# Kernel tuning notes

Measured on AMD Instinct MI355X. Metric: run time of the kernel, lower is better.

The kernel has to match this reference:

```python
import jax, jax.numpy as jnp
import numpy as np
from functools import partial

V, CTX, D, H, L, FF = 50257, 1024, 768, 12, 12, 3072
DH = D // H
EPS = 1e-5


def _ln(x, g, b):
    m = jnp.mean(x, axis=-1, keepdims=True)
    v = jnp.mean(jnp.square(x - m), axis=-1, keepdims=True)
    return (x - m) * jax.lax.rsqrt(v + EPS) * g + b


def setup_inputs() -> dict:
    key = jax.random.key(0)
    ks = jax.random.split(key, 8)
    s = 0.02
    return {
        "input_ids": jax.random.randint(ks[0], (2, 1024), 0, V),
        "token_emb": jax.random.normal(ks[1], (V, D), jnp.float32) * s,
        "pos_emb": jax.random.normal(ks[2], (CTX, D), jnp.float32) * s,
        "ln1_g": jnp.ones((L, D), jnp.float32),
        "ln1_b": jnp.zeros((L, D), jnp.float32),
        "qkv_w": jax.random.normal(ks[3], (L, 3 * D, D), jnp.float32) * s,
        "out_w": jax.random.normal(ks[4], (L, D, D), jnp.float32) * (s / np.sqrt(2 * L)),
        "ln2_g": jnp.ones((L, D), jnp.float32),
        "ln2_b": jnp.zeros((L, D), jnp.float32),
        "ff1_w": jax.random.normal(ks[5], (L, FF, D), jnp.float32) * s,
        "ff2_w": jax.random.normal(ks[6], (L, D, FF), jnp.float32) * s,
        "lnf_g": jnp.ones((D,), jnp.float32),
        "lnf_b": jnp.zeros((D,), jnp.float32),
    }


def reference(input_ids, token_emb, pos_emb, ln1_g, ln1_b, qkv_w, out_w,
              ln2_g, ln2_b, ff1_w, ff2_w, lnf_g, lnf_b):
    B, T = input_ids.shape
    x = token_emb[input_ids] + pos_emb[:T]  # [B,T,D]
    causal = jnp.tril(jnp.ones((T, T), bool))  # True = keep
    scale = 1.0 / np.sqrt(DH)

    def block(x, p):
        g1, b1, wqkv, wo, g2, b2, w1, w2 = p
        h = _ln(x, g1, b1)
        qkv = h @ wqkv.T  # [B,T,3D]
        q, k, v = jnp.split(qkv, 3, axis=-1)
        q = q.reshape(B, T, H, DH).transpose(0, 2, 1, 3)
        k = k.reshape(B, T, H, DH).transpose(0, 2, 1, 3)
        v = v.reshape(B, T, H, DH).transpose(0, 2, 1, 3)
        scores = jnp.einsum('bhqd,bhkd->bhqk', q, k) * scale
        scores = jnp.where(causal, scores, -jnp.inf)
        w = jax.nn.softmax(scores, axis=-1)
        o = jnp.einsum('bhqk,bhkd->bhqd', w, v)
        o = o.transpose(0, 2, 1, 3).reshape(B, T, D) @ wo.T
        x = x + o
        h2 = _ln(x, g2, b2)
        ff = jax.nn.gelu(h2 @ w1.T, approximate=False) @ w2.T
        return x + ff, None

    params = (ln1_g, ln1_b, qkv_w, out_w, ln2_g, ln2_b, ff1_w, ff2_w)
    x, _ = jax.lax.scan(block, x, params)
    x = _ln(x, lnf_g, lnf_b)
    logits = x @ token_emb.T  # tied lm head
    return logits
```

## Files before the change

kernel.cpp:

```cpp
#include <hip/hip_runtime.h>
#include <hip/hip_bf16.h>
#include <math.h>

#define D_MODEL 768
#define NHEAD 12
#define DHEAD 64
#define NLAYER 12
#define FF_DIM 3072
#define SEQ 1024
#define TOKENS 2048
#define VOCAB 50257

typedef short bf16x8 __attribute__((ext_vector_type(8)));
typedef float f32x4 __attribute__((ext_vector_type(4)));
typedef unsigned short u16x4 __attribute__((ext_vector_type(4)));
typedef unsigned short u16x8 __attribute__((ext_vector_type(8)));

__device__ inline unsigned short f2bf(float f) {
    union { float f; unsigned u; } un;
    un.f = f;
    unsigned u = un.u;
    u += 0x7fffu + ((u >> 16) & 1u);
    return (unsigned short)(u >> 16);
}

__device__ inline void gl_lds16(const void* g, void* l) {
    __builtin_amdgcn_global_load_lds(
        (const __attribute__((address_space(1))) unsigned int*)g,
        (__attribute__((address_space(3))) unsigned int*)l, 16, 0, 0);
}

__global__ __launch_bounds__(256) void cvt_kernel(const float* __restrict__ s,
                                                  unsigned short* __restrict__ d,
                                                  long n4) {
    long i = (long)blockIdx.x * 256 + threadIdx.x;
    long stride = (long)gridDim.x * 256;
    for (; i < n4; i += stride) {
        f32x4 v = ((const f32x4*)s)[i];
        u16x4 r;
        r[0] = f2bf(v[0]); r[1] = f2bf(v[1]); r[2] = f2bf(v[2]); r[3] = f2bf(v[3]);
        ((u16x4*)d)[i] = r;
    }
}

__global__ __launch_bounds__(256) void embed_kernel(const int* __restrict__ ids,
                                                    const float* __restrict__ tok,
                                                    const float* __restrict__ pos,
                                                    float* __restrict__ x) {
    int i = blockIdx.x * 256 + threadIdx.x;
    int row = i / D_MODEL;
    int d = i - row * D_MODEL;
    int t = row & (SEQ - 1);
    x[i] = tok[(long)ids[row] * D_MODEL + d] + pos[(long)t * D_MODEL + d];
}

__global__ __launch_bounds__(256) void ln_kernel(const float* __restrict__ x,
                                                 const float* __restrict__ g,
                                                 const float* __restrict__ b,
                                                 unsigned short* __restrict__ out) {
    int row = blockIdx.x;
    int tid = threadIdx.x;
    const float* xr = x + (long)row * D_MODEL;
    float v0 = xr[tid], v1 = xr[tid + 256], v2 = xr[tid + 512];
    __shared__ float sm[4];
    float s = v0 + v1 + v2;
    #pragma unroll
    for (int off = 32; off; off >>= 1) s += __shfl_xor(s, off);
    if ((tid & 63) == 0) sm[tid >> 6] = s;
    __syncthreads();
    float mean = (sm[0] + sm[1] + sm[2] + sm[3]) * (1.f / D_MODEL);
    __syncthreads();
    float d0 = v0 - mean, d1 = v1 - mean, d2 = v2 - mean;
    s = d0 * d0 + d1 * d1 + d2 * d2;
    #pragma unroll
    for (int off = 32; off; off >>= 1) s += __shfl_xor(s, off);
    if ((tid & 63) == 0) sm[tid >> 6] = s;
    __syncthreads();
    float var = (sm[0] + sm[1] + sm[2] + sm[3]) * (1.f / D_MODEL);
    float rs = rsqrtf(var + 1e-5f);
    unsigned short* orow = out + (long)row * D_MODEL;
    orow[tid]       = f2bf(d0 * rs * g[tid]       + b[tid]);
    orow[tid + 256] = f2bf(d1 * rs * g[tid + 256] + b[tid + 256]);
    orow[tid + 512] = f2bf(d2 * rs * g[tid + 512] + b[tid + 512]);
}

#define GM_NONE 0
#define GM_RES  1
#define GM_GELU 2
#define GM_QKV  3

template<int WM, int WN, int MODE, bool SWZ>
__global__ __launch_bounds__(256) void gemm_bf16(
        const unsigned short* __restrict__ A, const unsigned short* __restrict__ W,
        int M, int N, int K,
        float* __restrict__ Cf, unsigned short* __restrict__ Cb,
        const float* __restrict__ RES,
        unsigned short* __restrict__ P1, unsigned short* __restrict__ P2) {
    constexpr int BM = WM * 32, BN = WN * 32;
    __shared__ unsigned short lA[2][BM * 64];
    __shared__ unsigned short lB[2][BN * 64];

    int tid = threadIdx.x;
    int lane = tid & 63, wv = tid >> 6;
    int wr = wv >> 1, wc = wv & 1;
    int lr = lane & 15, kq = lane >> 4;

    int mtile, ntile;
    if (SWZ) {
        int lb = blockIdx.y * gridDim.x + blockIdx.x;
        int g = lb >> 3, r8 = lb & 7;
        mtile = g % gridDim.x;
        ntile = (g / gridDim.x) * 8 + r8;
        if (ntile * BN >= N) return;
    } else {
        mtile = blockIdx.x;
        ntile = blockIdx.y;
    }
    int row0 = mtile * BM;
    int col0 = ntile * BN;

    int srow_in = tid >> 3;
    int ssp = tid & 7;
    int skg = ssp ^ (srow_in & 7);
    int lbase = ((tid & ~63)) << 3;

    f32x4 acc[WM][WN];
    #pragma unroll
    for (int m = 0; m < WM; m++)
        #pragma unroll
        for (int n = 0; n < WN; n++) acc[m][n] = (f32x4){0.f, 0.f, 0.f, 0.f};

    auto stage = [&](int buf, int kt) {
        #pragma unroll
        for (int i = 0; i < BM / 32; i++) {
            int row = i * 32 + srow_in;
            gl_lds16(A + (size_t)(row0 + row) * K + kt + skg * 8,
                     &lA[buf][i * 2048 + lbase]);
        }
        #pragma unroll
        for (int i = 0; i < BN / 32; i++) {
            int row = i * 32 + srow_in;
            int srow = col0 + row;
            if (srow >= N) srow = N - 1;
            gl_lds16(W + (size_t)srow * K + kt + skg * 8,
                     &lB[buf][i * 2048 + lbase]);
        }
    };

    stage(0, 0);
    __syncthreads();
    int nt = K >> 6;
    int cur = 0;
    for (int t = 0; t < nt; t++) {
        if (t + 1 < nt) stage(cur ^ 1, (t + 1) << 6);
        #pragma unroll
        for (int kk = 0; kk < 2; kk++) {
            int kg = kk * 4 + kq;
            bf16x8 af[WM], bfr[WN];
            #pragma unroll
            for (int m = 0; m < WM; m++) {
                int row = wr * (WM * 16) + m * 16 + lr;
                af[m] = *(const bf16x8*)&lA[cur][row * 64 + ((kg ^ (row & 7)) << 3)];
            }
            #pragma unroll
            for (int n = 0; n < WN; n++) {
                int row = wc * (WN * 16) + n * 16 + lr;
                bfr[n] = *(const bf16x8*)&lB[cur][row * 64 + ((kg ^ (row & 7)) << 3)];
            }
            #pragma unroll
            for (int m = 0; m < WM; m++)
                #pragma unroll
                for (int n = 0; n < WN; n++)
                    acc[m][n] = __builtin_amdgcn_mfma_f32_16x16x32_bf16(af[m], bfr[n], acc[m][n], 0, 0, 0);
        }
        __syncthreads();
        cur ^= 1;
    }

    #pragma unroll
    for (int m = 0; m < WM; m++) {
        int r0 = row0 + wr * (WM * 16) + m * 16 + (kq << 2);
        #pragma unroll
        for (int n = 0; n < WN; n++) {
            int c = col0 + wc * (WN * 16) + n * 16 + lr;
            if (c < N) {
                #pragma unroll
                for (int j = 0; j < 4; j++) {
                    int r = r0 + j;
                    size_t idx = (size_t)r * N + c;
                    float v = acc[m][n][j];
                    if (MODE == GM_RES) {
                        Cf[idx] = v + RES[idx];
                    } else if (MODE == GM_GELU) {
                        Cb[idx] = f2bf(0.5f * v * (1.f + erff(v * 0.70710678118f)));
                    } else if (MODE == GM_QKV) {
                        int bb = r >> 10, t = r & 1023;
                        if (c < D_MODEL) {
                            int h = c >> 6, dh = c & 63;
                            P1[(((size_t)(bb * NHEAD + h) * SEQ) + t) * 64 + dh] = f2bf(v * 0.125f);
                        } else if (c < 2 * D_MODEL) {
                            int cc = c - D_MODEL;
                            int h = cc >> 6, dh = cc & 63;
                            P2[(((size_t)(bb * NHEAD + h) * SEQ) + t) * 64 + dh] = f2bf(v);
                        } else {
                            Cb[(size_t)r * D_MODEL + (c - 2 * D_MODEL)] = f2bf(v);
                        }
                    } else {
                        Cf[idx] = v;
                    }
                }
            }
        }
    }
}

__global__ __launch_bounds__(256) void vprep_kernel(const unsigned short* __restrict__ Vrow,
                                                    unsigned short* __restrict__ Vt) {
    __shared__ unsigned short T[64][66];
    int b = blockIdx.z, h = blockIdx.y, t0 = blockIdx.x * 64;
    int tid = threadIdx.x;
    int tin = tid >> 2, seg = tid & 3;
    const unsigned short* src = Vrow + ((size_t)(b * SEQ) + t0 + tin) * D_MODEL
                                + h * 64 + seg * 16;
    u16x8 a0 = *(const u16x8*)src;
    u16x8 a1 = *(const u16x8*)(src + 8);
    #pragma unroll
    for (int e = 0; e < 8; e++) { T[tin][seg * 16 + e] = a0[e]; T[tin][seg * 16 + 8 + e] = a1[e]; }
    __syncthreads();
    int dh = tid >> 2;
    unsigned short* dst = Vt + ((size_t)(b * NHEAD + h) * 64 + dh) * SEQ + t0 + seg * 16;
    u16x8 o0, o1;
    #pragma unroll
    for (int e = 0; e < 8; e++) o0[e] = T[seg * 16 + e][dh];
    #pragma unroll
    for (int e = 0; e < 8; e++) o1[e] = T[seg * 16 + 8 + e][dh];
    *(u16x8*)dst = o0;
    *(u16x8*)(dst + 8) = o1;
}

__global__ __launch_bounds__(128) void attn_mfma(const unsigned short* __restrict__ Qb,
                                                 const unsigned short* __restrict__ Kb,
                                                 const unsigned short* __restrict__ Vt,
                                                 unsigned short* __restrict__ att) {
    int b = blockIdx.z, h = blockIdx.y, pr = blockIdx.x;
    int tid = threadIdx.x, l = tid & 63, w = tid >> 6;
    int lr = l & 15, hg = l >> 4;
    int hk8 = hg * 8, hg4 = hg * 4;
    size_t bh = (size_t)b * NHEAD + h;
    const unsigned short* Qp = Qb + bh * SEQ * 64;
    const unsigned short* Kp = Kb + bh * SEQ * 64;
    const unsigned short* Vp = Vt + bh * 64 * SEQ;

    __shared__ float sm_m[2][2][16], sm_l[2][2][16];
    __shared__ float sm_o[2][2][16][64];
    __shared__ unsigned short pl[2][1024];
    unsigned short* Pw = &pl[w][0];

    #pragma unroll
    for (int ti = 0; ti < 2; ti++) {
        int tile = ti ? (63 - pr) : pr;
        int q0 = tile * 16;
        bf16x8 qf0 = *(const bf16x8*)(Qp + (size_t)(q0 + lr) * 64 + hk8);
        bf16x8 qf1 = *(const bf16x8*)(Qp + (size_t)(q0 + lr) * 64 + 32 + hk8);
        f32x4 O[4];
        #pragma unroll
        for (int dt = 0; dt < 4; dt++) O[dt] = (f32x4){0.f, 0.f, 0.f, 0.f};
        f32x4 mrun = (f32x4){-1e30f, -1e30f, -1e30f, -1e30f};
        f32x4 lrun = (f32x4){0.f, 0.f, 0.f, 0.f};
        int nch = (tile >> 2) + 1;

        for (int c = w; c < nch; c += 2) {
            int k0 = c * 64;
            f32x4 S[4];
            #pragma unroll
            for (int kt = 0; kt < 4; kt++) {
                S[kt] = (f32x4){0.f, 0.f, 0.f, 0.f};
                bf16x8 kf = *(const bf16x8*)(Kp + (size_t)(k0 + kt * 16 + lr) * 64 + hk8);
                S[kt] = __builtin_amdgcn_mfma_f32_16x16x32_bf16(qf0, kf, S[kt], 0, 0, 0);
                kf = *(const bf16x8*)(Kp + (size_t)(k0 + kt * 16 + lr) * 64 + 32 + hk8);
                S[kt] = __builtin_amdgcn_mfma_f32_16x16x32_bf16(qf1, kf, S[kt], 0, 0, 0);
            }
            if (c == nch - 1) {
                #pragma unroll
                for (int kt = 0; kt < 4; kt++)
                    #pragma unroll
                    for (int j = 0; j < 4; j++)
                        S[kt][j] = (k0 + kt * 16 + lr <= q0 + hg4 + j) ? S[kt][j] : -3.0e38f;
            }
            f32x4 rm;
            #pragma unroll
            for (int j = 0; j < 4; j++)
                rm[j] = fmaxf(fmaxf(S[0][j], S[1][j]), fmaxf(S[2][j], S[3][j]));
            #pragma unroll
            for (int msk = 1; msk <= 8; msk <<= 1)
                #pragma unroll
                for (int j = 0; j < 4; j++)
                    rm[j] = fmaxf(rm[j], __shfl_xor(rm[j], msk));
            f32x4 mn, corr, rs;
            #pragma unroll
            for (int j = 0; j < 4; j++) {
                mn[j] = fmaxf(mrun[j], rm[j]);
                corr[j] = __expf(mrun[j] - mn[j]);
                rs[j] = 0.f;
            }
            #pragma unroll
            for (int kt = 0; kt < 4; kt++)
                #pragma unroll
                for (int j = 0; j < 4; j++) {
                    float p = __expf(S[kt][j] - mn[j]);
                    S[kt][j] = p;
                    rs[j] += p;
                }
            #pragma unroll
            for (int msk = 1; msk <= 8; msk <<= 1)
                #pragma unroll
                for (int j = 0; j < 4; j++)
                    rs[j] += __shfl_xor(rs[j], msk);
            #pragma unroll
            for (int j = 0; j < 4; j++) {
                lrun[j] = lrun[j] * corr[j] + rs[j];
                mrun[j] = mn[j];
            }
            #pragma unroll
            for (int dt = 0; dt < 4; dt++)
                #pragma unroll
                for (int j = 0; j < 4; j++) O[dt][j] *= corr[j];
            #pragma unroll
            for (int kt = 0; kt < 4; kt++) {
                int cc = kt * 16 + lr;
                int slot = cc >> 3, off = cc & 7;
                #pragma unroll
                for (int j = 0; j < 4; j++) {
                    int r = hg4 + j;
                    Pw[r * 64 + ((slot ^ (r & 7)) << 3) + off] = f2bf(S[kt][j]);
                }
            }
            asm volatile("s_waitcnt lgkmcnt(0)" ::: "memory");
            bf16x8 pf0 = *(const bf16x8*)&Pw[lr * 64 + ((hg ^ (lr & 7)) << 3)];
            bf16x8 pf1 = *(const bf16x8*)&Pw[lr * 64 + (((4 + hg) ^ (lr & 7)) << 3)];
            #pragma unroll
            for (int dt = 0; dt < 4; dt++) {
                bf16x8 vf = *(const bf16x8*)(Vp + (size_t)(dt * 16 + lr) * SEQ + k0 + hk8);
                O[dt] = __builtin_amdgcn_mfma_f32_16x16x32_bf16(pf0, vf, O[dt], 0, 0, 0);
                vf = *(const bf16x8*)(Vp + (size_t)(dt * 16 + lr) * SEQ + k0 + 32 + hk8);
                O[dt] = __builtin_amdgcn_mfma_f32_16x16x32_bf16(pf1, vf, O[dt], 0, 0, 0);
            }
        }
        if (lr == 0) {
            #pragma unroll
            for (int j = 0; j < 4; j++) {
                sm_m[w][ti][hg4 + j] = mrun[j];
                sm_l[w][ti][hg4 + j] = lrun[j];
            }
        }
        #pragma unroll
        for (int dt = 0; dt < 4; dt++)
            #pragma unroll
            for (int j = 0; j < 4; j++)
                sm_o[w][ti][hg4 + j][dt * 16 + lr] = O[dt][j];
    }
    __syncthreads();
    {
        int tile = w ? (63 - pr) : pr;
        int q0 = tile * 16;
        #pragma unroll
        for (int j = 0; j < 4; j++) {
            int r = hg4 + j;
            float m0 = sm_m[0][w][r], m1 = sm_m[1][w][r];
            float M = fmaxf(m0, m1);
            float e0 = __expf(m0 - M), e1 = __expf(m1 - M);
            float L = sm_l[0][w][r] * e0 + sm_l[1][w][r] * e1;
            float invL = 1.f / L;
            unsigned short* orow = att + ((size_t)(b * SEQ + q0 + r)) * D_MODEL + h * 64;
            #pragma unroll
            for (int dt = 0; dt < 4; dt++) {
                float o = sm_o[0][w][r][dt * 16 + lr] * e0 + sm_o[1][w][r][dt * 16 + lr] * e1;
                orow[dt * 16 + lr] = f2bf(o * invL);
            }
        }
    }
}

extern "C" void kernel_launch(void* const* d_in, const int* in_sizes, int n_in,
                              void* d_out, int out_size, void* d_ws, size_t ws_size,
                              hipStream_t stream) {
    const int*   input_ids = (const int*)d_in[0];
    const float* token_emb = (const float*)d_in[1];
    const float* pos_emb   = (const float*)d_in[2];
    const float* ln1_g     = (const float*)d_in[3];
    const float* ln1_b     = (const float*)d_in[4];
    const float* qkv_w     = (const float*)d_in[5];
    const float* out_w     = (const float*)d_in[6];
    const float* ln2_g     = (const float*)d_in[7];
    const float* ln2_b     = (const float*)d_in[8];
    const float* ff1_w     = (const float*)d_in[9];
    const float* ff2_w     = (const float*)d_in[10];
    const float* lnf_g     = (const float*)d_in[11];
    const float* lnf_b     = (const float*)d_in[12];
    float* out = (float*)d_out;

    const size_t SZ_QKV_L = (size_t)3 * D_MODEL * D_MODEL;
    const size_t SZ_OUT_L = (size_t)D_MODEL * D_MODEL;
    const size_t SZ_FF1_L = (size_t)FF_DIM * D_MODEL;
    const size_t SZ_FF2_L = (size_t)D_MODEL * FF_DIM;
    const size_t SZ_TOK   = (size_t)VOCAB * D_MODEL;

    char* base = (char*)d_ws;
    size_t off = 0;
    auto alloc = [&](size_t bytes) -> char* {
        char* p = base + off;
        off = (off + bytes + 255) & ~(size_t)255;
        return p;
    };

    float* x              = (float*)alloc((size_t)TOKENS * D_MODEL * 4);
    unsigned short* hb    = (unsigned short*)alloc((size_t)TOKENS * D_MODEL * 2);
    unsigned short* attb  = (unsigned short*)alloc((size_t)TOKENS * D_MODEL * 2);
    unsigned short* ffab  = (unsigned short*)alloc((size_t)TOKENS * FF_DIM * 2);
    unsigned short* Qb    = (unsigned short*)alloc((size_t)TOKENS * D_MODEL * 2);
    unsigned short* Kb    = (unsigned short*)alloc((size_t)TOKENS * D_MODEL * 2);
    unsigned short* Vrow  = (unsigned short*)alloc((size_t)TOKENS * D_MODEL * 2);
    unsigned short* Vtb   = (unsigned short*)alloc((size_t)TOKENS * D_MODEL * 2);

    size_t act_end = off;
    size_t full_need = act_end + 2 * (NLAYER * (SZ_QKV_L + SZ_OUT_L + SZ_FF1_L + SZ_FF2_L) + SZ_TOK)
                       + 6 * 256;
    bool full = ws_size >= full_need;

    unsigned short *qkvA, *outA, *ff1A, *ff2A, *tokA;
    if (full) {
        qkvA = (unsigned short*)alloc(2 * NLAYER * SZ_QKV_L);
        outA = (unsigned short*)alloc(2 * NLAYER * SZ_OUT_L);
        ff1A = (unsigned short*)alloc(2 * NLAYER * SZ_FF1_L);
        ff2A = (unsigned short*)alloc(2 * NLAYER * SZ_FF2_L);
        tokA = (unsigned short*)alloc(2 * SZ_TOK);
    } else {
        qkvA = (unsigned short*)alloc(2 * SZ_QKV_L);
        outA = (unsigned short*)alloc(2 * SZ_OUT_L);
        ff1A = (unsigned short*)alloc(2 * SZ_FF1_L);
        ff2A = (unsigned short*)alloc(2 * SZ_FF2_L);
        tokA = (unsigned short*)alloc(2 * SZ_TOK);
    }

    auto cvt = [&](const float* s, unsigned short* d, size_t n) {
        long n4 = (long)(n / 4);
        int g = (int)((n4 + 255) / 256);
        if (g > 2048) g = 2048;
        cvt_kernel<<<g, 256, 0, stream>>>(s, d, n4);
    };

    if (full) {
        cvt(qkv_w, qkvA, NLAYER * SZ_QKV_L);
        cvt(out_w, outA, NLAYER * SZ_OUT_L);
        cvt(ff1_w, ff1A, NLAYER * SZ_FF1_L);
        cvt(ff2_w, ff2A, NLAYER * SZ_FF2_L);
        cvt(token_emb, tokA, SZ_TOK);
    }

    embed_kernel<<<TOKENS * D_MODEL / 256, 256, 0, stream>>>(input_ids, token_emb, pos_emb, x);

    for (int l = 0; l < NLAYER; l++) {
        const unsigned short* qw = full ? qkvA + (size_t)l * SZ_QKV_L : qkvA;
        const unsigned short* ow = full ? outA + (size_t)l * SZ_OUT_L : outA;
        const unsigned short* f1 = full ? ff1A + (size_t)l * SZ_FF1_L : ff1A;
        const unsigned short* f2 = full ? ff2A + (size_t)l * SZ_FF2_L : ff2A;

        ln_kernel<<<TOKENS, 256, 0, stream>>>(x, ln1_g + l * D_MODEL, ln1_b + l * D_MODEL, hb);
        if (!full) cvt(qkv_w + (size_t)l * SZ_QKV_L, qkvA, SZ_QKV_L);
        gemm_bf16<4, 4, GM_QKV, false><<<dim3(TOKENS / 128, 3 * D_MODEL / 128), 256, 0, stream>>>(
            hb, qw, TOKENS, 3 * D_MODEL, D_MODEL, nullptr, Vrow, nullptr, Qb, Kb);
        vprep_kernel<<<dim3(SEQ / 64, NHEAD, 2), 256, 0, stream>>>(Vrow, Vtb);
        attn_mfma<<<dim3(32, NHEAD, 2), 128, 0, stream>>>(Qb, Kb, Vtb, attb);
        if (!full) cvt(out_w + (size_t)l * SZ_OUT_L, outA, SZ_OUT_L);
        gemm_bf16<2, 4, GM_RES, false><<<dim3(TOKENS / 64, D_MODEL / 128), 256, 0, stream>>>(
            attb, ow, TOKENS, D_MODEL, D_MODEL, x, nullptr, x, nullptr, nullptr);
        ln_kernel<<<TOKENS, 256, 0, stream>>>(x, ln2_g + l * D_MODEL, ln2_b + l * D_MODEL, hb);
        if (!full) cvt(ff1_w + (size_t)l * SZ_FF1_L, ff1A, SZ_FF1_L);
        gemm_bf16<4, 4, GM_GELU, false><<<dim3(TOKENS / 128, FF_DIM / 128), 256, 0, stream>>>(
            hb, f1, TOKENS, FF_DIM, D_MODEL, nullptr, ffab, nullptr, nullptr, nullptr);
        if (!full) cvt(ff2_w + (size_t)l * SZ_FF2_L, ff2A, SZ_FF2_L);
        gemm_bf16<2, 4, GM_RES, false><<<dim3(TOKENS / 64, D_MODEL / 128), 256, 0, stream>>>(
            ffab, f2, TOKENS, D_MODEL, FF_DIM, x, nullptr, x, nullptr, nullptr);
    }

    ln_kernel<<<TOKENS, 256, 0, stream>>>(x, lnf_g, lnf_b, hb);
    if (!full) cvt(token_emb, tokA, SZ_TOK);
    gemm_bf16<4, 4, GM_NONE, true><<<dim3(TOKENS / 128, 400), 256, 0, stream>>>(
        hb, tokA, TOKENS, VOCAB, D_MODEL, out, nullptr, nullptr, nullptr, nullptr);
}
```

Measured before the change: 2.479 ms.

## Single-buffer GEMM LDS, widen attention to four waves, shrink QKV/FF1 tiles

```diff
diff --git a/kernel.cpp b/kernel.cpp
--- a/kernel.cpp
+++ b/kernel.cpp
@@ -97,8 +97,8 @@
         const float* __restrict__ RES,
         unsigned short* __restrict__ P1, unsigned short* __restrict__ P2) {
     constexpr int BM = WM * 32, BN = WN * 32;
-    __shared__ unsigned short lA[2][BM * 64];
-    __shared__ unsigned short lB[2][BN * 64];
+    __shared__ unsigned short lA[BM * 64];
+    __shared__ unsigned short lB[BN * 64];
 
     int tid = threadIdx.x;
     int lane = tid & 63, wv = tid >> 6;
@@ -130,12 +130,12 @@
         #pragma unroll
         for (int n = 0; n < WN; n++) acc[m][n] = (f32x4){0.f, 0.f, 0.f, 0.f};
 
-    auto stage = [&](int buf, int kt) {
+    for (int kt = 0; kt < K; kt += 64) {
         #pragma unroll
         for (int i = 0; i < BM / 32; i++) {
             int row = i * 32 + srow_in;
             gl_lds16(A + (size_t)(row0 + row) * K + kt + skg * 8,
-                     &lA[buf][i * 2048 + lbase]);
+                     &lA[i * 2048 + lbase]);
         }
         #pragma unroll
         for (int i = 0; i < BN / 32; i++) {
@@ -143,16 +143,9 @@
             int srow = col0 + row;
             if (srow >= N) srow = N - 1;
             gl_lds16(W + (size_t)srow * K + kt + skg * 8,
-                     &lB[buf][i * 2048 + lbase]);
-        }
-    };
-
-    stage(0, 0);
-    __syncthreads();
-    int nt = K >> 6;
-    int cur = 0;
-    for (int t = 0; t < nt; t++) {
-        if (t + 1 < nt) stage(cur ^ 1, (t + 1) << 6);
+                     &lB[i * 2048 + lbase]);
+        }
+        __syncthreads();
         #pragma unroll
         for (int kk = 0; kk < 2; kk++) {
             int kg = kk * 4 + kq;
@@ -160,12 +153,12 @@
             #pragma unroll
             for (int m = 0; m < WM; m++) {
                 int row = wr * (WM * 16) + m * 16 + lr;
-                af[m] = *(const bf16x8*)&lA[cur][row * 64 + ((kg ^ (row & 7)) << 3)];
+                af[m] = *(const bf16x8*)&lA[row * 64 + ((kg ^ (row & 7)) << 3)];
             }
             #pragma unroll
             for (int n = 0; n < WN; n++) {
                 int row = wc * (WN * 16) + n * 16 + lr;
-                bfr[n] = *(const bf16x8*)&lB[cur][row * 64 + ((kg ^ (row & 7)) << 3)];
+                bfr[n] = *(const bf16x8*)&lB[row * 64 + ((kg ^ (row & 7)) << 3)];
             }
             #pragma unroll
             for (int m = 0; m < WM; m++)
@@ -174,7 +167,6 @@
                     acc[m][n] = __builtin_amdgcn_mfma_f32_16x16x32_bf16(af[m], bfr[n], acc[m][n], 0, 0, 0);
         }
         __syncthreads();
-        cur ^= 1;
     }
 
     #pragma unroll
@@ -238,7 +230,8 @@
     *(u16x8*)(dst + 8) = o1;
 }
 
-__global__ __launch_bounds__(128) void attn_mfma(const unsigned short* __restrict__ Qb,
+#define ANW 4
+__global__ __launch_bounds__(256) void attn_mfma(const unsigned short* __restrict__ Qb,
                                                  const unsigned short* __restrict__ Kb,
                                                  const unsigned short* __restrict__ Vt,
                                                  unsigned short* __restrict__ att) {
@@ -251,9 +244,9 @@
     const unsigned short* Kp = Kb + bh * SEQ * 64;
     const unsigned short* Vp = Vt + bh * 64 * SEQ;
 
-    __shared__ float sm_m[2][2][16], sm_l[2][2][16];
-    __shared__ float sm_o[2][2][16][64];
-    __shared__ unsigned short pl[2][1024];
+    __shared__ float sm_m[ANW][2][16], sm_l[ANW][2][16];
+    __shared__ float sm_o[ANW][2][16][65];
+    __shared__ unsigned short pl[ANW][1024];
     unsigned short* Pw = &pl[w][0];
 
     #pragma unroll
@@ -269,7 +262,7 @@
         f32x4 lrun = (f32x4){0.f, 0.f, 0.f, 0.f};
         int nch = (tile >> 2) + 1;
 
-        for (int c = w; c < nch; c += 2) {
+        for (int c = w; c < nch; c += ANW) {
             int k0 = c * 64;
             f32x4 S[4];
             #pragma unroll
@@ -361,21 +354,28 @@
     }
     __syncthreads();
     {
-        int tile = w ? (63 - pr) : pr;
+        int ti2 = w >> 1;
+        int tile = ti2 ? (63 - pr) : pr;
         int q0 = tile * 16;
         #pragma unroll
-        for (int j = 0; j < 4; j++) {
+        for (int jj = 0; jj < 2; jj++) {
+            int j = (w & 1) * 2 + jj;
             int r = hg4 + j;
-            float m0 = sm_m[0][w][r], m1 = sm_m[1][w][r];
-            float M = fmaxf(m0, m1);
+            float m0 = sm_m[0][ti2][r], m1 = sm_m[1][ti2][r];
+            float m2 = sm_m[2][ti2][r], m3 = sm_m[3][ti2][r];
+            float M = fmaxf(fmaxf(m0, m1), fmaxf(m2, m3));
             float e0 = __expf(m0 - M), e1 = __expf(m1 - M);
-            float L = sm_l[0][w][r] * e0 + sm_l[1][w][r] * e1;
+            float e2 = __expf(m2 - M), e3 = __expf(m3 - M);
+            float L = sm_l[0][ti2][r] * e0 + sm_l[1][ti2][r] * e1
+                    + sm_l[2][ti2][r] * e2 + sm_l[3][ti2][r] * e3;
             float invL = 1.f / L;
             unsigned short* orow = att + ((size_t)(b * SEQ + q0 + r)) * D_MODEL + h * 64;
             #pragma unroll
             for (int dt = 0; dt < 4; dt++) {
-                float o = sm_o[0][w][r][dt * 16 + lr] * e0 + sm_o[1][w][r][dt * 16 + lr] * e1;
-                orow[dt * 16 + lr] = f2bf(o * invL);
+                int cidx = dt * 16 + lr;
+                float o = sm_o[0][ti2][r][cidx] * e0 + sm_o[1][ti2][r][cidx] * e1
+                        + sm_o[2][ti2][r][cidx] * e2 + sm_o[3][ti2][r][cidx] * e3;
+                orow[cidx] = f2bf(o * invL);
             }
         }
     }
@@ -467,16 +467,16 @@
 
         ln_kernel<<<TOKENS, 256, 0, stream>>>(x, ln1_g + l * D_MODEL, ln1_b + l * D_MODEL, hb);
         if (!full) cvt(qkv_w + (size_t)l * SZ_QKV_L, qkvA, SZ_QKV_L);
-        gemm_bf16<4, 4, GM_QKV, false><<<dim3(TOKENS / 128, 3 * D_MODEL / 128), 256, 0, stream>>>(
+        gemm_bf16<2, 4, GM_QKV, false><<<dim3(TOKENS / 64, 3 * D_MODEL / 128), 256, 0, stream>>>(
             hb, qw, TOKENS, 3 * D_MODEL, D_MODEL, nullptr, Vrow, nullptr, Qb, Kb);
         vprep_kernel<<<dim3(SEQ / 64, NHEAD, 2), 256, 0, stream>>>(Vrow, Vtb);
-        attn_mfma<<<dim3(32, NHEAD, 2), 128, 0, stream>>>(Qb, Kb, Vtb, attb);
+        attn_mfma<<<dim3(32, NHEAD, 2), 256, 0, stream>>>(Qb, Kb, Vtb, attb);
         if (!full) cvt(out_w + (size_t)l * SZ_OUT_L, outA, SZ_OUT_L);
         gemm_bf16<2, 4, GM_RES, false><<<dim3(TOKENS / 64, D_MODEL / 128), 256, 0, stream>>>(
             attb, ow, TOKENS, D_MODEL, D_MODEL, x, nullptr, x, nullptr, nullptr);
         ln_kernel<<<TOKENS, 256, 0, stream>>>(x, ln2_g + l * D_MODEL, ln2_b + l * D_MODEL, hb);
         if (!full) cvt(ff1_w + (size_t)l * SZ_FF1_L, ff1A, SZ_FF1_L);
-        gemm_bf16<4, 4, GM_GELU, false><<<dim3(TOKENS / 128, FF_DIM / 128), 256, 0, stream>>>(
+        gemm_bf16<2, 4, GM_GELU, false><<<dim3(TOKENS / 64, FF_DIM / 128), 256, 0, stream>>>(
             hb, f1, TOKENS, FF_DIM, D_MODEL, nullptr, ffab, nullptr, nullptr, nullptr);
         if (!full) cvt(ff2_w + (size_t)l * SZ_FF2_L, ff2A, SZ_FF2_L);
         gemm_bf16<2, 4, GM_RES, false><<<dim3(TOKENS / 64, D_MODEL / 128), 256, 0, stream>>>(
```

Result: faster. 2.417 ms (-2.5%).
